# Optimization experiments

Hardware: AMD Instinct MI355X
Metric: run time of the kernel (lower is better)

## Reference

```python
import math
import jax, jax.numpy as jnp
import numpy as np

SQ, SK, B, D = 2048, 2048, 4, 512


def setup_inputs() -> dict:
    key = jax.random.key(0)
    kq, kk, kv = jax.random.split(key, 3)
    Q = jax.random.normal(kq, (SQ, B, D), dtype=jnp.float32)
    K = jax.random.normal(kk, (SK, B, D), dtype=jnp.float32)
    V = jax.random.normal(kv, (SK, B, D), dtype=jnp.float32)
    key_mask = jnp.zeros((SK, B), dtype=bool)  # True = masked key
    return {"Q": Q, "K": K, "V": V, "key_mask": key_mask}


def reference(Q, K, V, key_mask):
    # Layout: [seq, batch, d]. scores: [Sq, B, Sk]
    d = K.shape[2]
    scores = jnp.einsum('ibd,kbd->ibk', Q, K) / math.sqrt(d)
    Sq, Bb, Sk = scores.shape
    # causal mask: disallow k > i
    causal = jnp.triu(jnp.ones((Sq, Sk), dtype=bool), k=1)[:, None, :]
    neg_inf = jnp.array(-jnp.inf, dtype=scores.dtype)
    scores = jnp.where(causal, neg_inf, scores)
    # key padding mask: key_mask [Sk, B] -> [1, B, Sk]
    scores = jnp.where(key_mask.T[None, :, :], neg_inf, scores)
    p = jax.nn.softmax(scores, axis=2)
    return jnp.einsum('ibk,kbd->ibd', p, V)
```

## Files before the change

kernel.cpp:

```cpp
#include <hip/hip_runtime.h>

#define SEQ   2048
#define BATCH 4
#define DIM   512
#define VAOFF 65536
#define PAOFF 131072
#define LDS_TOTAL 139264
#define NEG_INF  (-__builtin_inff())

typedef short short8 __attribute__((ext_vector_type(8)));
typedef float floatx4 __attribute__((ext_vector_type(4)));

using lds_char = __attribute__((address_space(3))) char;
using g_void   = const __attribute__((address_space(1))) void;
using l_void   = __attribute__((address_space(3))) void;

__device__ __forceinline__ short to_bf16(float x){
    unsigned u = __float_as_uint(x);
    unsigned r = (u + 0x7fffu + ((u >> 16) & 1u)) >> 16;
    return (short)r;
}

__device__ __forceinline__ short8 pack8(floatx4 a, floatx4 b, float s){
    short8 r;
    r[0]=to_bf16(a[0]*s); r[1]=to_bf16(a[1]*s); r[2]=to_bf16(a[2]*s); r[3]=to_bf16(a[3]*s);
    r[4]=to_bf16(b[0]*s); r[5]=to_bf16(b[1]*s); r[6]=to_bf16(b[2]*s); r[7]=to_bf16(b[7-7]*s);
    return r;
}

__device__ __forceinline__ short8 pack8f(floatx4 a, floatx4 b, float s){
    short8 r;
    r[0]=to_bf16(a[0]*s); r[1]=to_bf16(a[1]*s); r[2]=to_bf16(a[2]*s); r[3]=to_bf16(a[3]*s);
    r[4]=to_bf16(b[0]*s); r[5]=to_bf16(b[1]*s); r[6]=to_bf16(b[2]*s); r[7]=to_bf16(b[3]*s);
    return r;
}

extern "C" __global__ void __launch_bounds__(256)
conv_k(const float* __restrict__ K, short* __restrict__ Kimg)
{
    const int t    = blockIdx.x * 256 + threadIdx.x;
    const int d8   = t & 63;
    const int row  = t >> 6;
    const int k    = row >> 2;
    const int b    = row & 3;
    const float* src = K + (size_t)row * DIM + d8 * 8;
    floatx4 f0 = *(const floatx4*)src;
    floatx4 f1 = *(const floatx4*)(src + 4);
    const int slot = (d8 * 8) ^ ((k & 7) << 3);
    *(short8*)(Kimg + ((size_t)b * SEQ + k) * DIM + slot) = pack8f(f0, f1, 1.0f);
}

extern "C" __global__ void __launch_bounds__(256)
conv_v(const float* __restrict__ V, short* __restrict__ Vt)
{
    const int t    = blockIdx.x * 256 + threadIdx.x;
    const int dv   = t & 511;
    const int rest = t >> 9;
    const int kc   = rest & 255;
    const int b    = rest >> 8;
    short8 colv;
    #pragma unroll
    for (int i = 0; i < 8; ++i){
        const float f = V[((size_t)(kc*8 + i) * BATCH + b) * DIM + dv];
        colv[i] = to_bf16(f);
    }
    *(short8*)(Vt + ((size_t)b * DIM + dv) * SEQ + kc * 8) = colv;
}

extern "C" __global__ void __launch_bounds__(256)
merge_o(const float* __restrict__ partO, const float* __restrict__ stats,
        float* __restrict__ Og)
{
    const int t = blockIdx.x * 256 + threadIdx.x;
    const int d = t & 511;
    const int u = t >> 9;
    const int b = u & 3;
    const int v = u >> 2;
    const int qt = v >> 5;
    const int r  = v & 31;
    const int p0 = (qt*4 + b)*2;
    const float O0 = partO[((size_t)p0*32 + r)*512 + d];
    const float O1 = partO[((size_t)(p0+1)*32 + r)*512 + d];
    const float m0 = stats[p0*64 + r],     l0 = stats[p0*64 + 32 + r];
    const float m1 = stats[(p0+1)*64 + r], l1 = stats[(p0+1)*64 + 32 + r];
    const float M  = fmaxf(m0, m1);
    const float a0 = (m0 == NEG_INF) ? 0.f : __expf(m0 - M);
    const float a1 = (m1 == NEG_INF) ? 0.f : __expf(m1 - M);
    const float l  = a0*l0 + a1*l1;
    const float inv = (l > 0.f) ? 1.0f/l : 0.f;
    Og[((size_t)v*BATCH + b)*DIM + d] = (a0*O0 + a1*O1) * inv;
}

extern "C" __global__ void __launch_bounds__(512, 1)
fa_fwd(const float* __restrict__ Qg, const short* __restrict__ Kb,
       const short* __restrict__ Vt, const unsigned char* __restrict__ Mg,
       float* __restrict__ partO, float* __restrict__ stats)
{
    extern __shared__ __align__(16) char smem[];
    const int tid  = threadIdx.x;
    const int w    = tid >> 6;
    const int lane = tid & 63;
    const int g    = lane >> 4;
    const int c    = lane & 15;
    const int qhalf = w & 1;
    const int dvq   = w >> 1;

    const int slot = blockIdx.x & 7;
    const int b    = slot >> 1;
    const int h    = slot & 1;
    const int s    = blockIdx.x >> 3;

    const int cntA  = (s + 2 - h) >> 1;
    const int cntB  = (65 - s - h) >> 1;
    const int total = cntA + cntB;

    const short* Kbb = Kb + (size_t)b * SEQ * DIM;
    const short* Vtb = Vt + (size_t)b * DIM * SEQ;

    char* Pb = smem + PAOFF + w*1024;

    #define STAGE(tt, dd) { \
        if (w < 4){ \
            const short* ksrc_ = Kbb + ((size_t)((tt)*32 + w*8)) * DIM + lane*8; \
            char* dst_ = smem + (dd)*32768 + w*8192; \
            _Pragma("unroll") \
            for (int i2 = 0; i2 < 8; ++i2) \
                __builtin_amdgcn_global_load_lds((g_void*)(ksrc_ + (size_t)i2*DIM), \
                    (l_void*)(lds_char*)(dst_ + i2*1024), 16, 0, 0); \
        } else { \
            const int u_ = w - 4, j_ = u_ >> 1, hi_ = u_ & 1; \
            char* dst_ = smem + VAOFF + (dd)*32768 + j_*16384 + hi_*8192; \
            _Pragma("unroll") \
            for (int i2 = 0; i2 < 8; ++i2){ \
                const int iv_ = hi_*8 + i2; \
                const short* vsrc_ = Vtb + (size_t)(iv_*32 + (lane>>1))*SEQ \
                                   + (tt)*32 + j_*16 + (lane&1)*8; \
                __builtin_amdgcn_global_load_lds((g_void*)vsrc_, \
                    (l_void*)(lds_char*)(dst_ + i2*1024), 16, 0, 0); } \
        } }

    #define TILE_OF(j) ((j) < cntA ? (h + 2*(j)) : (h + 2*((j) - cntA)))

    const float scale = 0.04419417382415922f;
    short8 qreg[16];
    floatx4 oacc[8];
    float mrow[4], lrow[4];
    int qt_cur = s;

    {
        const float* qrow = Qg + ((size_t)(s*32 + qhalf*16 + c) * BATCH + b) * DIM + g * 8;
        #pragma unroll
        for (int ks = 0; ks < 16; ++ks){
            floatx4 f0 = *(const floatx4*)(qrow + ks*32);
            floatx4 f1 = *(const floatx4*)(qrow + ks*32 + 4);
            qreg[ks] = pack8f(f0, f1, scale);
        }
    }
    #pragma unroll
    for (int i=0;i<8;++i){ floatx4 z = {0.f,0.f,0.f,0.f}; oacc[i]=z; }
    #pragma unroll
    for (int jj=0;jj<4;++jj){ mrow[jj] = NEG_INF; lrow[jj] = 0.f; }

    STAGE(TILE_OF(0), 0);

    #pragma unroll 1
    for (int j = 0; j < total; ++j){

        if (j == cntA){
            const int inst = (s*4 + b)*2 + h;
            float* po = partO + (size_t)inst * 32 * 512;
            #pragma unroll
            for (int nt = 0; nt < 8; ++nt){
                #pragma unroll
                for (int jj = 0; jj < 4; ++jj)
                    po[(size_t)(qhalf*16 + g*4 + jj)*512 + dvq*128 + nt*16 + c] = oacc[nt][jj];
            }
            if (dvq == 0 && c == 0){
                #pragma unroll
                for (int jj = 0; jj < 4; ++jj){
                    const int R = qhalf*16 + g*4 + jj;
                    stats[inst*64 + R]      = mrow[jj];
                    stats[inst*64 + 32 + R] = lrow[jj];
                }
            }
            qt_cur = 63 - s;
            const float* qrow = Qg + ((size_t)(qt_cur*32 + qhalf*16 + c) * BATCH + b) * DIM + g * 8;
            #pragma unroll
            for (int ks = 0; ks < 16; ++ks){
                floatx4 f0 = *(const floatx4*)(qrow + ks*32);
                floatx4 f1 = *(const floatx4*)(qrow + ks*32 + 4);
                qreg[ks] = pack8f(f0, f1, scale);
            }
            #pragma unroll
            for (int i=0;i<8;++i){ floatx4 z = {0.f,0.f,0.f,0.f}; oacc[i]=z; }
            #pragma unroll
            for (int jj=0;jj<4;++jj){ mrow[jj] = NEG_INF; lrow[jj] = 0.f; }
        }

        const int d  = j & 1;
        const int kb = TILE_OF(j) * 32;
        const int qrow0 = qt_cur*32 + qhalf*16;

        asm volatile("s_waitcnt vmcnt(0)" ::: "memory");
        __syncthreads();

        if (j + 1 < total) STAGE(TILE_OF(j+1), d ^ 1);

        const char* kb_ = smem + d*32768;
        const char* vb_ = smem + VAOFF + d*32768;

        const unsigned char km0 = Mg[(kb + c) * BATCH + b];
        const unsigned char km1 = Mg[(kb + 16 + c) * BATCH + b];

        floatx4 sacc[2];
        { floatx4 z = {0.f,0.f,0.f,0.f}; sacc[0]=z; sacc[1]=z; }
        #pragma unroll
        for (int ks = 0; ks < 16; ++ks){
            #pragma unroll
            for (int jcol = 0; jcol < 2; ++jcol){
                short8 kf = *(const short8*)(kb_ + jcol*16384 + c*1024 +
                               ((ks*64 + g*16) ^ ((c & 7) << 4)));
                sacc[jcol] = __builtin_amdgcn_mfma_f32_16x16x32_bf16(qreg[ks], kf, sacc[jcol], 0,0,0);
            }
        }

        float sv[2][4];
        #pragma unroll
        for (int jcol = 0; jcol < 2; ++jcol){
            const int col = kb + jcol*16 + c;
            const unsigned char km = jcol ? km1 : km0;
            #pragma unroll
            for (int jj = 0; jj < 4; ++jj){
                const int row = qrow0 + g*4 + jj;
                sv[jcol][jj] = (col > row || km) ? NEG_INF : sacc[jcol][jj];
            }
        }
        float pmax[4];
        #pragma unroll
        for (int jj=0;jj<4;++jj) pmax[jj] = fmaxf(sv[0][jj], sv[1][jj]);
        #pragma unroll
        for (int msk=1; msk<16; msk<<=1){
            #pragma unroll
            for (int jj=0;jj<4;++jj)
                pmax[jj] = fmaxf(pmax[jj], __shfl_xor(pmax[jj], msk, 64));
        }
        const bool okd = (pmax[0] <= mrow[0]+8.f) && (pmax[1] <= mrow[1]+8.f)
                      && (pmax[2] <= mrow[2]+8.f) && (pmax[3] <= mrow[3]+8.f);
        if (!__all(okd)){
            float fsc[4];
            #pragma unroll
            for (int jj=0;jj<4;++jj){
                const float M = fmaxf(mrow[jj], pmax[jj]);
                const float f = (mrow[jj] == NEG_INF) ? 0.f : __expf(mrow[jj] - M);
                mrow[jj] = M; lrow[jj] *= f; fsc[jj] = f;
            }
            #pragma unroll
            for (int nt=0; nt<8; ++nt){
                #pragma unroll
                for (int jj=0; jj<4; ++jj) oacc[nt][jj] *= fsc[jj];
            }
        }
        float parr[2][4], psum[4] = {0.f,0.f,0.f,0.f};
        #pragma unroll
        for (int jcol=0; jcol<2; ++jcol){
            #pragma unroll
            for (int jj=0; jj<4; ++jj){
                const float x = sv[jcol][jj];
                const float e = (x == NEG_INF) ? 0.f : __expf(x - mrow[jj]);
                parr[jcol][jj] = e; psum[jj] += e;
            }
        }
        #pragma unroll
        for (int msk=1; msk<16; msk<<=1){
            #pragma unroll
            for (int jj=0;jj<4;++jj) psum[jj] += __shfl_xor(psum[jj], msk, 64);
        }
        #pragma unroll
        for (int jj=0;jj<4;++jj) lrow[jj] += psum[jj];

        #pragma unroll
        for (int jcol=0; jcol<2; ++jcol){
            #pragma unroll
            for (int jj=0; jj<4; ++jj)
                *(short*)(Pb + (g*4 + jj)*64 + (jcol*16 + c)*2) = to_bf16(parr[jcol][jj]);
        }

        const short8 pfrag = *(const short8*)(Pb + c*64 + g*16);
        #pragma unroll
        for (int nt = 0; nt < 8; ++nt){
            const int dv = dvq*128 + nt*16 + c;
            const short8 vfr = *(const short8*)(vb_ + (g>>1)*16384 + dv*32 + (g&1)*16);
            oacc[nt] = __builtin_amdgcn_mfma_f32_16x16x32_bf16(pfrag, vfr, oacc[nt], 0,0,0);
        }
    }

    {
        const int inst = ((63 - s)*4 + b)*2 + h;
        float* po = partO + (size_t)inst * 32 * 512;
        #pragma unroll
        for (int nt = 0; nt < 8; ++nt){
            #pragma unroll
            for (int jj = 0; jj < 4; ++jj)
                po[(size_t)(qhalf*16 + g*4 + jj)*512 + dvq*128 + nt*16 + c] = oacc[nt][jj];
        }
        if (dvq == 0 && c == 0){
            #pragma unroll
            for (int jj = 0; jj < 4; ++jj){
                const int R = qhalf*16 + g*4 + jj;
                stats[inst*64 + R]      = mrow[jj];
                stats[inst*64 + 32 + R] = lrow[jj];
            }
        }
    }
    #undef STAGE
    #undef TILE_OF
}

extern "C" void kernel_launch(void* const* d_in, const int* in_sizes, int n_in,
                              void* d_out, int out_size, void* d_ws, size_t ws_size,
                              hipStream_t stream)
{
    const float* Q = (const float*)d_in[0];
    const float* K = (const float*)d_in[1];
    const float* V = (const float*)d_in[2];
    const unsigned char* M = (const unsigned char*)d_in[3];
    float* O = (float*)d_out;
    (void)in_sizes; (void)n_in; (void)out_size; (void)ws_size;

    short* Kb    = (short*)d_ws;
    short* Vt    = Kb + (size_t)BATCH * SEQ * DIM;
    float* partO = (float*)(Vt + (size_t)BATCH * SEQ * DIM);
    float* stats = partO + (size_t)512 * 32 * 512;

    conv_k<<<2048, 256, 0, stream>>>(K, Kb);
    conv_v<<<2048, 256, 0, stream>>>(V, Vt);

    hipFuncSetAttribute(reinterpret_cast<const void*>(fa_fwd),
                        hipFuncAttributeMaxDynamicSharedMemorySize, LDS_TOTAL);
    fa_fwd<<<256, 512, LDS_TOTAL, stream>>>(Q, Kb, Vt, M, partO, stats);

    merge_o<<<16384, 256, 0, stream>>>(partO, stats, O);
}
```

Baseline: 138.6 us.

## Split fa_fwd into 16-row query blocks of 256 threads and read V from global

The attention kernel now runs 512 blocks of 4 waves, each covering 16 query rows, instead of 256 blocks of 8 waves covering 32 rows, with two blocks allowed per CU. V is no longer staged in LDS. Each wave loads its V fragments straight from global memory into registers, so LDS use drops to about 66 KB and the staging step handles only K. The aim is higher occupancy and less LDS pressure, at the cost of loading each K tile twice (once per 16-row block) and V reads that bypass LDS and may stall the PV MFMAs.

```diff
diff --git a/kernel.cpp b/kernel.cpp
--- a/kernel.cpp
+++ b/kernel.cpp
@@ -3,9 +3,8 @@
 #define SEQ   2048
 #define BATCH 4
 #define DIM   512
-#define VAOFF 65536
-#define PAOFF 131072
-#define LDS_TOTAL 139264
+#define POFF  65536
+#define LDS_TOTAL 67584
 #define NEG_INF  (-__builtin_inff())
 
 typedef short short8 __attribute__((ext_vector_type(8)));
@@ -19,13 +18,6 @@
     unsigned u = __float_as_uint(x);
     unsigned r = (u + 0x7fffu + ((u >> 16) & 1u)) >> 16;
     return (short)r;
-}
-
-__device__ __forceinline__ short8 pack8(floatx4 a, floatx4 b, float s){
-    short8 r;
-    r[0]=to_bf16(a[0]*s); r[1]=to_bf16(a[1]*s); r[2]=to_bf16(a[2]*s); r[3]=to_bf16(a[3]*s);
-    r[4]=to_bf16(b[0]*s); r[5]=to_bf16(b[1]*s); r[6]=to_bf16(b[2]*s); r[7]=to_bf16(b[7-7]*s);
-    return r;
 }
 
 __device__ __forceinline__ short8 pack8f(floatx4 a, floatx4 b, float s){
@@ -73,16 +65,16 @@
 {
     const int t = blockIdx.x * 256 + threadIdx.x;
     const int d = t & 511;
-    const int u = t >> 9;
-    const int b = u & 3;
-    const int v = u >> 2;
-    const int qt = v >> 5;
-    const int r  = v & 31;
-    const int p0 = (qt*4 + b)*2;
-    const float O0 = partO[((size_t)p0*32 + r)*512 + d];
-    const float O1 = partO[((size_t)(p0+1)*32 + r)*512 + d];
-    const float m0 = stats[p0*64 + r],     l0 = stats[p0*64 + 32 + r];
-    const float m1 = stats[(p0+1)*64 + r], l1 = stats[(p0+1)*64 + 32 + r];
+    const int uu = t >> 9;
+    const int b = uu & 3;
+    const int v = uu >> 2;
+    const int v16 = v >> 4;
+    const int r   = v & 15;
+    const int p0  = (v16*4 + b)*2;
+    const float O0 = partO[((size_t)p0*16 + r)*512 + d];
+    const float O1 = partO[((size_t)(p0+1)*16 + r)*512 + d];
+    const float m0 = stats[p0*32 + r],     l0 = stats[p0*32 + 16 + r];
+    const float m1 = stats[(p0+1)*32 + r], l1 = stats[(p0+1)*32 + 16 + r];
     const float M  = fmaxf(m0, m1);
     const float a0 = (m0 == NEG_INF) ? 0.f : __expf(m0 - M);
     const float a1 = (m1 == NEG_INF) ? 0.f : __expf(m1 - M);
@@ -91,7 +83,7 @@
     Og[((size_t)v*BATCH + b)*DIM + d] = (a0*O0 + a1*O1) * inv;
 }
 
-extern "C" __global__ void __launch_bounds__(512, 1)
+extern "C" __global__ void __launch_bounds__(256, 2)
 fa_fwd(const float* __restrict__ Qg, const short* __restrict__ Kb,
        const short* __restrict__ Vt, const unsigned char* __restrict__ Mg,
        float* __restrict__ partO, float* __restrict__ stats)
@@ -102,13 +94,13 @@
     const int lane = tid & 63;
     const int g    = lane >> 4;
     const int c    = lane & 15;
-    const int qhalf = w & 1;
-    const int dvq   = w >> 1;
 
     const int slot = blockIdx.x & 7;
     const int b    = slot >> 1;
     const int h    = slot & 1;
-    const int s    = blockIdx.x >> 3;
+    const int idx  = blockIdx.x >> 3;
+    const int u    = idx & 1;
+    const int s    = idx >> 1;
 
     const int cntA  = (s + 2 - h) >> 1;
     const int cntB  = (65 - s - h) >> 1;
@@ -116,28 +108,15 @@
 
     const short* Kbb = Kb + (size_t)b * SEQ * DIM;
     const short* Vtb = Vt + (size_t)b * DIM * SEQ;
-
-    char* Pb = smem + PAOFF + w*1024;
+    char* Pb = smem + POFF;
 
     #define STAGE(tt, dd) { \
-        if (w < 4){ \
-            const short* ksrc_ = Kbb + ((size_t)((tt)*32 + w*8)) * DIM + lane*8; \
-            char* dst_ = smem + (dd)*32768 + w*8192; \
-            _Pragma("unroll") \
-            for (int i2 = 0; i2 < 8; ++i2) \
-                __builtin_amdgcn_global_load_lds((g_void*)(ksrc_ + (size_t)i2*DIM), \
-                    (l_void*)(lds_char*)(dst_ + i2*1024), 16, 0, 0); \
-        } else { \
-            const int u_ = w - 4, j_ = u_ >> 1, hi_ = u_ & 1; \
-            char* dst_ = smem + VAOFF + (dd)*32768 + j_*16384 + hi_*8192; \
-            _Pragma("unroll") \
-            for (int i2 = 0; i2 < 8; ++i2){ \
-                const int iv_ = hi_*8 + i2; \
-                const short* vsrc_ = Vtb + (size_t)(iv_*32 + (lane>>1))*SEQ \
-                                   + (tt)*32 + j_*16 + (lane&1)*8; \
-                __builtin_amdgcn_global_load_lds((g_void*)vsrc_, \
-                    (l_void*)(lds_char*)(dst_ + i2*1024), 16, 0, 0); } \
-        } }
+        const short* ksrc_ = Kbb + ((size_t)((tt)*32 + w*8)) * DIM + lane*8; \
+        char* dst_ = smem + (dd)*32768 + w*8192; \
+        _Pragma("unroll") \
+        for (int i2 = 0; i2 < 8; ++i2) \
+            __builtin_amdgcn_global_load_lds((g_void*)(ksrc_ + (size_t)i2*DIM), \
+                (l_void*)(lds_char*)(dst_ + i2*1024), 16, 0, 0); }
 
     #define TILE_OF(j) ((j) < cntA ? (h + 2*(j)) : (h + 2*((j) - cntA)))
 
@@ -148,7 +127,7 @@
     int qt_cur = s;
 
     {
-        const float* qrow = Qg + ((size_t)(s*32 + qhalf*16 + c) * BATCH + b) * DIM + g * 8;
+        const float* qrow = Qg + ((size_t)((s*2+u)*16 + c) * BATCH + b) * DIM + g * 8;
         #pragma unroll
         for (int ks = 0; ks < 16; ++ks){
             floatx4 f0 = *(const floatx4*)(qrow + ks*32);
@@ -167,24 +146,23 @@
     for (int j = 0; j < total; ++j){
 
         if (j == cntA){
-            const int inst = (s*4 + b)*2 + h;
-            float* po = partO + (size_t)inst * 32 * 512;
+            const int inst = ((s*2 + u)*4 + b)*2 + h;
+            float* po = partO + (size_t)inst * 16 * 512;
             #pragma unroll
             for (int nt = 0; nt < 8; ++nt){
                 #pragma unroll
                 for (int jj = 0; jj < 4; ++jj)
-                    po[(size_t)(qhalf*16 + g*4 + jj)*512 + dvq*128 + nt*16 + c] = oacc[nt][jj];
-            }
-            if (dvq == 0 && c == 0){
+                    po[(size_t)(g*4 + jj)*512 + w*128 + nt*16 + c] = oacc[nt][jj];
+            }
+            if (w == 0 && c == 0){
                 #pragma unroll
                 for (int jj = 0; jj < 4; ++jj){
-                    const int R = qhalf*16 + g*4 + jj;
-                    stats[inst*64 + R]      = mrow[jj];
-                    stats[inst*64 + 32 + R] = lrow[jj];
+                    stats[inst*32 + g*4 + jj]      = mrow[jj];
+                    stats[inst*32 + 16 + g*4 + jj] = lrow[jj];
                 }
             }
             qt_cur = 63 - s;
-            const float* qrow = Qg + ((size_t)(qt_cur*32 + qhalf*16 + c) * BATCH + b) * DIM + g * 8;
+            const float* qrow = Qg + ((size_t)((qt_cur*2+u)*16 + c) * BATCH + b) * DIM + g * 8;
             #pragma unroll
             for (int ks = 0; ks < 16; ++ks){
                 floatx4 f0 = *(const floatx4*)(qrow + ks*32);
@@ -197,9 +175,9 @@
             for (int jj=0;jj<4;++jj){ mrow[jj] = NEG_INF; lrow[jj] = 0.f; }
         }
 
-        const int d  = j & 1;
-        const int kb = TILE_OF(j) * 32;
-        const int qrow0 = qt_cur*32 + qhalf*16;
+        const int d     = j & 1;
+        const int kb    = TILE_OF(j) * 32;
+        const int qrow0 = (qt_cur*2 + u) * 16;
 
         asm volatile("s_waitcnt vmcnt(0)" ::: "memory");
         __syncthreads();
@@ -207,10 +185,16 @@
         if (j + 1 < total) STAGE(TILE_OF(j+1), d ^ 1);
 
         const char* kb_ = smem + d*32768;
-        const char* vb_ = smem + VAOFF + d*32768;
 
         const unsigned char km0 = Mg[(kb + c) * BATCH + b];
         const unsigned char km1 = Mg[(kb + 16 + c) * BATCH + b];
+
+        short8 vf[8];
+        #pragma unroll
+        for (int nt = 0; nt < 8; ++nt){
+            const int dv = w*128 + nt*16 + c;
+            vf[nt] = *(const short8*)(Vtb + (size_t)dv * SEQ + kb + g*8);
+        }
 
         floatx4 sacc[2];
         { floatx4 z = {0.f,0.f,0.f,0.f}; sacc[0]=z; sacc[1]=z; }
@@ -288,27 +272,24 @@
         const short8 pfrag = *(const short8*)(Pb + c*64 + g*16);
         #pragma unroll
         for (int nt = 0; nt < 8; ++nt){
-            const int dv = dvq*128 + nt*16 + c;
-            const short8 vfr = *(const short8*)(vb_ + (g>>1)*16384 + dv*32 + (g&1)*16);
-            oacc[nt] = __builtin_amdgcn_mfma_f32_16x16x32_bf16(pfrag, vfr, oacc[nt], 0,0,0);
+            oacc[nt] = __builtin_amdgcn_mfma_f32_16x16x32_bf16(pfrag, vf[nt], oacc[nt], 0,0,0);
         }
     }
 
     {
-        const int inst = ((63 - s)*4 + b)*2 + h;
-        float* po = partO + (size_t)inst * 32 * 512;
+        const int inst = ((qt_cur*2 + u)*4 + b)*2 + h;
+        float* po = partO + (size_t)inst * 16 * 512;
         #pragma unroll
         for (int nt = 0; nt < 8; ++nt){
             #pragma unroll
             for (int jj = 0; jj < 4; ++jj)
-                po[(size_t)(qhalf*16 + g*4 + jj)*512 + dvq*128 + nt*16 + c] = oacc[nt][jj];
-        }
-        if (dvq == 0 && c == 0){
+                po[(size_t)(g*4 + jj)*512 + w*128 + nt*16 + c] = oacc[nt][jj];
+        }
+        if (w == 0 && c == 0){
             #pragma unroll
             for (int jj = 0; jj < 4; ++jj){
-                const int R = qhalf*16 + g*4 + jj;
-                stats[inst*64 + R]      = mrow[jj];
-                stats[inst*64 + 32 + R] = lrow[jj];
+                stats[inst*32 + g*4 + jj]      = mrow[jj];
+                stats[inst*32 + 16 + g*4 + jj] = lrow[jj];
             }
         }
     }
@@ -330,14 +311,14 @@
     short* Kb    = (short*)d_ws;
     short* Vt    = Kb + (size_t)BATCH * SEQ * DIM;
     float* partO = (float*)(Vt + (size_t)BATCH * SEQ * DIM);
-    float* stats = partO + (size_t)512 * 32 * 512;
+    float* stats = partO + (size_t)1024 * 16 * 512;
 
     conv_k<<<2048, 256, 0, stream>>>(K, Kb);
     conv_v<<<2048, 256, 0, stream>>>(V, Vt);
 
     hipFuncSetAttribute(reinterpret_cast<const void*>(fa_fwd),
                         hipFuncAttributeMaxDynamicSharedMemorySize, LDS_TOTAL);
-    fa_fwd<<<256, 512, LDS_TOTAL, stream>>>(Q, Kb, Vt, M, partO, stats);
+    fa_fwd<<<512, 256, LDS_TOTAL, stream>>>(Q, Kb, Vt, M, partO, stats);
 
     merge_o<<<16384, 256, 0, stream>>>(partO, stats, O);
 }
```

New measurement: 141.1 us. Within noise of the previous version (+1.8%).
